# Performance work log

Hardware: AMD Instinct MI355X
Metric: run time of the kernel (lower is better)

The kernel has to match this reference:

```python
import jax, jax.numpy as jnp
import numpy as np

DIM = 2048
NH = 16
HD = DIM // NH  # 128


def setup_inputs() -> dict:
    key = jax.random.key(0)
    ks = jax.random.split(key, 9)
    s_in = 1.0 / np.sqrt(DIM)
    inp = {
        "x": jax.random.normal(ks[0], (2, 2048, DIM), dtype=jnp.float32),
        # torch Linear weights stored as (out, in); we keep (in, out) for x @ W
        "wq": jax.random.uniform(ks[1], (DIM, DIM), jnp.float32, -s_in, s_in),
        "bq": jax.random.uniform(ks[2], (DIM,), jnp.float32, -s_in, s_in),
        "wk": jax.random.uniform(ks[3], (DIM, HD), jnp.float32, -s_in, s_in),
        "bk": jax.random.uniform(ks[4], (HD,), jnp.float32, -s_in, s_in),
        "wv": jax.random.uniform(ks[5], (DIM, HD), jnp.float32, -s_in, s_in),
        "bv": jax.random.uniform(ks[6], (HD,), jnp.float32, -s_in, s_in),
        "wo": jax.random.uniform(ks[7], (DIM, DIM), jnp.float32, -s_in, s_in),
        "bo": jax.random.uniform(ks[8], (DIM,), jnp.float32, -s_in, s_in),
    }
    return inp


def reference(x, wq, bq, wk, bk, wv, bv, wo, bo):
    bs, sl, dim = x.shape
    q = x @ wq + bq                      # [b, s, dim]
    k = x @ wk + bk                      # [b, s, hd] (single shared KV head)
    v = x @ wv + bv                      # [b, s, hd]
    q = q.reshape(bs, sl, NH, HD)        # [b, s, h, hd]
    scale = 1.0 / np.sqrt(HD).astype(np.float32)
    # scores: broadcast single KV head over all query heads
    attn = jnp.einsum('bshd,btd->bhst', q, k) * scale   # [b, h, s, s]
    att = jax.nn.softmax(attn, axis=-1)
    o = jnp.einsum('bhst,btd->bshd', att, v)            # [b, s, h, hd]
    o = o.reshape(bs, sl, dim)
    return o @ wo + bo
```

## Files before the change

### kernel.cpp

```cpp
#include <hip/hip_runtime.h>
#include <hip/hip_bf16.h>
#include <math.h>

#define DIM 2048
#define NH 16
#define HD 128
#define BATCH 2
#define SEQ 2048
#define TOKENS (BATCH * SEQ)
#define NQKV (DIM + 2 * HD)

typedef __attribute__((ext_vector_type(8))) _Float16 f16x8;
typedef __attribute__((ext_vector_type(4))) float f32x4;
typedef unsigned short u16;

__device__ __forceinline__ u16 f2h(float f) {
    union { _Float16 h; u16 u; } v; v.h = (_Float16)f; return v.u;
}
__device__ __forceinline__ void gll16(const void* g, void* l) {
    __builtin_amdgcn_global_load_lds(
        (const __attribute__((address_space(1))) unsigned int*)g,
        (__attribute__((address_space(3))) unsigned int*)l, 16, 0, 0);
}

#define KIDX(r, c) ((r) * 128 + (((((c) << 1)) ^ (((r) & 7) << 4)) >> 1))
#define VIDX(d, c) ((d) * 64  + (((((c) << 1)) ^ (((d) & 7) << 4)) >> 1))
#define PIDX(row, col) ((row) * 64 + \
    (((((col) << 1)) ^ (((((row) >> 2) & 3) ^ ((row) & 3)) << 5)) >> 1))

__global__ __launch_bounds__(256) void conv_f16(
    const float* __restrict__ in, u16* __restrict__ out)
{
    const int i = blockIdx.x * 256 + threadIdx.x;
    const float4 v = ((const float4*)in)[i];
    ushort4 h;
    h.x = f2h(v.x); h.y = f2h(v.y); h.z = f2h(v.z); h.w = f2h(v.w);
    ((ushort4*)out)[i] = h;
}

__global__ __launch_bounds__(256) void transpose_f16(
    const float* __restrict__ W, u16* __restrict__ T, int K, int N, int rowoff)
{
    __shared__ float tile[32][33];
    const int k0 = blockIdx.x * 32;
    const int n0 = blockIdx.y * 32;
    const int tid = threadIdx.x;
#pragma unroll
    for (int i = 0; i < 4; ++i) {
        const int idx = tid + i * 256;
        const int r = idx >> 5, c = idx & 31;
        tile[r][c] = W[(size_t)(k0 + r) * N + n0 + c];
    }
    __syncthreads();
#pragma unroll
    for (int i = 0; i < 4; ++i) {
        const int idx = tid + i * 256;
        const int r = idx >> 5, c = idx & 31;
        T[(size_t)(rowoff + n0 + r) * K + k0 + c] = f2h(tile[c][r]);
    }
}

__global__ __launch_bounds__(256) void concat_bias(
    const float* __restrict__ bq, const float* __restrict__ bk,
    const float* __restrict__ bv, float* __restrict__ bc)
{
    const int i = blockIdx.x * 256 + threadIdx.x;
    float v;
    if (i < DIM) v = bq[i];
    else if (i < DIM + HD) v = bk[i - DIM];
    else v = bv[i - DIM - HD];
    bc[i] = v;
}

template <int MODE>
__global__ __launch_bounds__(256) void gemm_f16(
    const u16* __restrict__ A, const u16* __restrict__ B,
    const float* __restrict__ bias, float* __restrict__ Cf,
    u16* __restrict__ qdst, u16* __restrict__ kdst, u16* __restrict__ vtdst,
    float scale)
{
    constexpr int BK = 32;
    __shared__ u16 lds[2][2 * 128 * BK];

    const int tid = threadIdx.x;
    const int wid = tid >> 6;
    const int lane = tid & 63;
    const int lr = lane & 15;
    const int lhi = lane >> 4;
    const int wr = wid >> 1, wc = wid & 1;
    const int bm = blockIdx.y * 128;
    const int bn = blockIdx.x * 128;

    f32x4 acc[4][4];
#pragma unroll
    for (int i = 0; i < 4; ++i)
#pragma unroll
        for (int j = 0; j < 4; ++j) acc[i][j] = (f32x4){0.f, 0.f, 0.f, 0.f};

#define STAGE(buf_, k0_)                                                      \
    {                                                                         \
        _Pragma("unroll")                                                     \
        for (int rr = 0; rr < 2; ++rr) {                                      \
            const int slot = rr * 256 + tid;                                  \
            const int row = slot >> 2;                                        \
            const int gch = ((slot & 3) ^ ((row >> 1) & 3)) * 8;              \
            char* lbase = (char*)lds[buf_] + (size_t)(rr * 256 + wid * 64) * 16; \
            gll16(A + (size_t)(bm + row) * DIM + (k0_) + gch, lbase);         \
            gll16(B + (size_t)(bn + row) * DIM + (k0_) + gch, lbase + 8192);  \
        }                                                                     \
    }

    STAGE(0, 0);
    __syncthreads();

    int cur = 0;
    for (int k0 = 0; k0 < DIM; k0 += BK) {
        if (k0 + BK < DIM) STAGE(cur ^ 1, k0 + BK);

        f16x8 a[4], b[4];
#pragma unroll
        for (int i = 0; i < 4; ++i) {
            const int mrow = wr * 64 + i * 16 + lr;
            const int nrow = wc * 64 + i * 16 + lr;
            a[i] = *(const f16x8*)&lds[cur][mrow * BK + ((lhi ^ ((mrow >> 1) & 3)) * 8)];
            b[i] = *(const f16x8*)&lds[cur][4096 + nrow * BK + ((lhi ^ ((nrow >> 1) & 3)) * 8)];
        }
        __builtin_amdgcn_s_setprio(1);
#pragma unroll
        for (int i = 0; i < 4; ++i)
#pragma unroll
            for (int j = 0; j < 4; ++j)
                acc[i][j] = __builtin_amdgcn_mfma_f32_16x16x32_f16(a[i], b[j], acc[i][j], 0, 0, 0);
        __builtin_amdgcn_s_setprio(0);
        __syncthreads();
        cur ^= 1;
    }
#undef STAGE

    const float alpha = (MODE == 0 && bn < DIM) ? scale : 1.0f;
    float bj[4];
#pragma unroll
    for (int j = 0; j < 4; ++j) bj[j] = bias[bn + wc * 64 + j * 16 + lr];

#pragma unroll
    for (int i = 0; i < 4; ++i) {
#pragma unroll
        for (int j = 0; j < 4; ++j) {
#pragma unroll
            for (int r = 0; r < 4; ++r) {
                const int row = bm + wr * 64 + i * 16 + lhi * 4 + r;
                const int col = bn + wc * 64 + j * 16 + lr;
                const float val = (acc[i][j][r] + bj[j]) * alpha;
                if (MODE == 1) {
                    Cf[(size_t)row * DIM + col] = val;
                } else if (bn < DIM) {
                    qdst[(size_t)row * DIM + col] = f2h(val);
                } else if (bn < DIM + HD) {
                    kdst[(size_t)row * HD + (col - DIM)] = f2h(val);
                } else {
                    vtdst[(size_t)(col - DIM - HD) * TOKENS + row] = f2h(val);
                }
            }
        }
    }
}

__global__ __launch_bounds__(256, 2) void mqa_attn_f16(
    const u16* __restrict__ Q, const u16* __restrict__ Kg,
    const u16* __restrict__ Vtg, u16* __restrict__ Oh)
{
    __shared__ __align__(16) u16 Ks[2][64 * 128];
    __shared__ __align__(16) u16 Vt[2][128 * 64];
    __shared__ __align__(16) u16 Ps[4][32 * 64];

    const int tid = threadIdx.x;
    const int wid = tid >> 6;
    const int lane = tid & 63;
    const int lr = lane & 15;
    const int lhi = lane >> 4;

    const int qt = blockIdx.x;
    const int h  = blockIdx.y;
    const int b  = blockIdx.z;
    const size_t bseq = (size_t)b * SEQ;
    const int q0 = qt * 128 + wid * 32;

    f16x8 qf[2][4];
#pragma unroll
    for (int mt = 0; mt < 2; ++mt) {
        const u16* qrow = Q + (bseq + q0 + mt * 16 + lr) * DIM + (size_t)h * HD;
#pragma unroll
        for (int kk = 0; kk < 4; ++kk)
            qf[mt][kk] = *(const f16x8*)(qrow + kk * 32 + lhi * 8);
    }

    f16x8 ones;
#pragma unroll
    for (int j = 0; j < 8; ++j) ones[j] = (_Float16)1.0f;

    f32x4 o[2][8];
#pragma unroll
    for (int mt = 0; mt < 2; ++mt)
#pragma unroll
        for (int dt = 0; dt < 8; ++dt) o[mt][dt] = (f32x4){0.f, 0.f, 0.f, 0.f};
    float m[2][4], lsum[2][4];
#pragma unroll
    for (int mt = 0; mt < 2; ++mt)
#pragma unroll
        for (int r = 0; r < 4; ++r) { m[mt][r] = -INFINITY; lsum[mt][r] = 0.f; }

#define STAGE_KV(buf_, t0_)                                                   \
    {                                                                         \
        _Pragma("unroll")                                                     \
        for (int i = 0; i < 4; ++i) {                                         \
            const int L = i * 256 + tid;                                      \
            char* kbase = (char*)&Ks[buf_][0] + (size_t)(i * 256 + wid * 64) * 16; \
            char* vbase = (char*)&Vt[buf_][0] + (size_t)(i * 256 + wid * 64) * 16; \
            const int krow = L >> 4, kc = (L & 15) ^ ((L >> 4) & 7);          \
            const int vrow = L >> 3, vc = (L & 7) ^ ((L >> 3) & 7);           \
            gll16(&Kg[(bseq + (t0_) + krow) * HD + kc * 8], kbase);           \
            gll16(&Vtg[(size_t)vrow * TOKENS + bseq + (t0_) + vc * 8], vbase);\
        }                                                                     \
    }

    STAGE_KV(0, 0);
    __syncthreads();

    int cur = 0;
    for (int t0 = 0; t0 < SEQ; t0 += 64) {
        if (t0 + 64 < SEQ) STAGE_KV(cur ^ 1, t0 + 64);

        f32x4 sc[2][4];
#pragma unroll
        for (int mt = 0; mt < 2; ++mt)
#pragma unroll
            for (int ct = 0; ct < 4; ++ct) sc[mt][ct] = (f32x4){0.f, 0.f, 0.f, 0.f};
        __builtin_amdgcn_s_setprio(1);
#pragma unroll
        for (int kk = 0; kk < 4; ++kk)
#pragma unroll
            for (int ct = 0; ct < 4; ++ct) {
                const f16x8 kf = *(const f16x8*)&Ks[cur][KIDX(ct * 16 + lr, kk * 32 + lhi * 8)];
                sc[0][ct] = __builtin_amdgcn_mfma_f32_16x16x32_f16(qf[0][kk], kf, sc[0][ct], 0, 0, 0);
                sc[1][ct] = __builtin_amdgcn_mfma_f32_16x16x32_f16(qf[1][kk], kf, sc[1][ct], 0, 0, 0);
            }
        __builtin_amdgcn_s_setprio(0);

        float al[2][4];
        bool need[2] = {false, false};
#pragma unroll
        for (int mt = 0; mt < 2; ++mt) {
            float pm[4];
#pragma unroll
            for (int r = 0; r < 4; ++r)
                pm[r] = fmaxf(fmaxf(sc[mt][0][r], sc[mt][1][r]),
                              fmaxf(sc[mt][2][r], sc[mt][3][r]));
#pragma unroll
            for (int msk = 1; msk < 16; msk <<= 1)
#pragma unroll
                for (int r = 0; r < 4; ++r)
                    pm[r] = fmaxf(pm[r], __shfl_xor(pm[r], msk, 64));
#pragma unroll
            for (int r = 0; r < 4; ++r) {
                if (pm[r] > m[mt][r] + 8.f) {
                    al[mt][r] = __expf(m[mt][r] - pm[r]);
                    m[mt][r] = pm[r];
                    need[mt] = true;
                } else {
                    al[mt][r] = 1.f;
                }
            }
#pragma unroll
            for (int ct = 0; ct < 4; ++ct)
#pragma unroll
                for (int r = 0; r < 4; ++r)
                    Ps[wid][PIDX(mt * 16 + lhi * 4 + r, ct * 16 + lr)] =
                        f2h(__expf(sc[mt][ct][r] - m[mt][r]));
            if (need[mt]) {
#pragma unroll
                for (int dt = 0; dt < 8; ++dt)
#pragma unroll
                    for (int r = 0; r < 4; ++r)
                        o[mt][dt][r] *= al[mt][r];
            }
        }

        f32x4 lacc[2];
        lacc[0] = (f32x4){0.f, 0.f, 0.f, 0.f};
        lacc[1] = (f32x4){0.f, 0.f, 0.f, 0.f};
        __builtin_amdgcn_s_setprio(1);
#pragma unroll
        for (int kk = 0; kk < 2; ++kk) {
            const f16x8 pa0 = *(const f16x8*)&Ps[wid][PIDX(lr, kk * 32 + lhi * 8)];
            const f16x8 pa1 = *(const f16x8*)&Ps[wid][PIDX(16 + lr, kk * 32 + lhi * 8)];
            lacc[0] = __builtin_amdgcn_mfma_f32_16x16x32_f16(pa0, ones, lacc[0], 0, 0, 0);
            lacc[1] = __builtin_amdgcn_mfma_f32_16x16x32_f16(pa1, ones, lacc[1], 0, 0, 0);
#pragma unroll
            for (int dt = 0; dt < 8; ++dt) {
                const f16x8 vb = *(const f16x8*)&Vt[cur][VIDX(dt * 16 + lr, kk * 32 + lhi * 8)];
                o[0][dt] = __builtin_amdgcn_mfma_f32_16x16x32_f16(pa0, vb, o[0][dt], 0, 0, 0);
                o[1][dt] = __builtin_amdgcn_mfma_f32_16x16x32_f16(pa1, vb, o[1][dt], 0, 0, 0);
            }
        }
        __builtin_amdgcn_s_setprio(0);
#pragma unroll
        for (int mt = 0; mt < 2; ++mt)
#pragma unroll
            for (int r = 0; r < 4; ++r)
                lsum[mt][r] = lsum[mt][r] * al[mt][r] + lacc[mt][r];

        __syncthreads();
        cur ^= 1;
    }
#undef STAGE_KV

#pragma unroll
    for (int mt = 0; mt < 2; ++mt)
#pragma unroll
        for (int r = 0; r < 4; ++r) {
            const float inv = 1.f / lsum[mt][r];
            u16* op = Oh + (bseq + q0 + mt * 16 + lhi * 4 + r) * DIM
                         + (size_t)h * HD + lr;
#pragma unroll
            for (int dt = 0; dt < 8; ++dt)
                op[dt * 16] = f2h(o[mt][dt][r] * inv);
        }
}

extern "C" void kernel_launch(void* const* d_in, const int* in_sizes, int n_in,
                              void* d_out, int out_size, void* d_ws, size_t ws_size,
                              hipStream_t stream) {
    const float* x  = (const float*)d_in[0];
    const float* wq = (const float*)d_in[1];
    const float* bq = (const float*)d_in[2];
    const float* wk = (const float*)d_in[3];
    const float* bk = (const float*)d_in[4];
    const float* wv = (const float*)d_in[5];
    const float* bv = (const float*)d_in[6];
    const float* wo = (const float*)d_in[7];
    const float* bo = (const float*)d_in[8];
    float* out = (float*)d_out;

    char* w = (char*)d_ws;
    u16* xh     = (u16*)w;                 w += (size_t)TOKENS * DIM * 2;
    u16* wcat   = (u16*)w;                 w += (size_t)NQKV * DIM * 2;
    u16* woT    = (u16*)w;                 w += (size_t)DIM * DIM * 2;
    u16* qb     = (u16*)w;                 w += (size_t)TOKENS * DIM * 2;
    u16* kb     = (u16*)w;                 w += (size_t)TOKENS * HD * 2;
    u16* vtb    = (u16*)w;                 w += (size_t)TOKENS * HD * 2;
    float* bc   = (float*)w;               w += 16384;
    u16* Oh = xh;

    const float scale = 0.08838834764831845f;
    const dim3 blk(256);

    conv_f16<<<TOKENS * DIM / 4 / 256, blk, 0, stream>>>(x, xh);
    transpose_f16<<<dim3(DIM / 32, DIM / 32), blk, 0, stream>>>(wq, wcat, DIM, DIM, 0);
    transpose_f16<<<dim3(DIM / 32, HD / 32), blk, 0, stream>>>(wk, wcat, DIM, HD, DIM);
    transpose_f16<<<dim3(DIM / 32, HD / 32), blk, 0, stream>>>(wv, wcat, DIM, HD, DIM + HD);
    transpose_f16<<<dim3(DIM / 32, DIM / 32), blk, 0, stream>>>(wo, woT, DIM, DIM, 0);
    concat_bias<<<NQKV / 256, blk, 0, stream>>>(bq, bk, bv, bc);

    gemm_f16<0><<<dim3(NQKV / 128, TOKENS / 128), blk, 0, stream>>>(
        xh, wcat, bc, nullptr, qb, kb, vtb, scale);

    mqa_attn_f16<<<dim3(SEQ / 128, NH, BATCH), blk, 0, stream>>>(qb, kb, vtb, Oh);

    gemm_f16<1><<<dim3(DIM / 128, TOKENS / 128), blk, 0, stream>>>(
        Oh, woT, bo, out, nullptr, nullptr, nullptr, 1.0f);
}
```

Baseline: 246.0 us.

## Transpose attention MFMAs to keep P in registers via permlane swaps

```diff
diff --git a/kernel.cpp b/kernel.cpp
--- a/kernel.cpp
+++ b/kernel.cpp
@@ -11,8 +11,12 @@
 #define NQKV (DIM + 2 * HD)
 
 typedef __attribute__((ext_vector_type(8))) _Float16 f16x8;
+typedef __attribute__((ext_vector_type(2))) _Float16 f16x2;
 typedef __attribute__((ext_vector_type(4))) float f32x4;
 typedef unsigned short u16;
+typedef unsigned int u32;
+
+typedef union { u32 d[4]; f16x8 v; } frag_u;
 
 __device__ __forceinline__ u16 f2h(float f) {
     union { _Float16 h; u16 u; } v; v.h = (_Float16)f; return v.u;
@@ -25,8 +29,6 @@
 
 #define KIDX(r, c) ((r) * 128 + (((((c) << 1)) ^ (((r) & 7) << 4)) >> 1))
 #define VIDX(d, c) ((d) * 64  + (((((c) << 1)) ^ (((d) & 7) << 4)) >> 1))
-#define PIDX(row, col) ((row) * 64 + \
-    (((((col) << 1)) ^ (((((row) >> 2) & 3) ^ ((row) & 3)) << 5)) >> 1))
 
 __global__ __launch_bounds__(256) void conv_f16(
     const float* __restrict__ in, u16* __restrict__ out)
@@ -171,13 +173,13 @@
 {
     __shared__ __align__(16) u16 Ks[2][64 * 128];
     __shared__ __align__(16) u16 Vt[2][128 * 64];
-    __shared__ __align__(16) u16 Ps[4][32 * 64];
 
     const int tid = threadIdx.x;
     const int wid = tid >> 6;
     const int lane = tid & 63;
     const int lr = lane & 15;
     const int lhi = lane >> 4;
+    const bool l5 = (lhi & 2) != 0;
 
     const int qt = blockIdx.x;
     const int h  = blockIdx.y;
@@ -203,11 +205,8 @@
     for (int mt = 0; mt < 2; ++mt)
 #pragma unroll
         for (int dt = 0; dt < 8; ++dt) o[mt][dt] = (f32x4){0.f, 0.f, 0.f, 0.f};
-    float m[2][4], lsum[2][4];
-#pragma unroll
-    for (int mt = 0; mt < 2; ++mt)
-#pragma unroll
-        for (int r = 0; r < 4; ++r) { m[mt][r] = -INFINITY; lsum[mt][r] = 0.f; }
+    float m[2]    = {-INFINITY, -INFINITY};
+    float lsum[2] = {0.f, 0.f};
 
 #define STAGE_KV(buf_, t0_)                                                   \
     {                                                                         \
@@ -241,48 +240,62 @@
 #pragma unroll
             for (int ct = 0; ct < 4; ++ct) {
                 const f16x8 kf = *(const f16x8*)&Ks[cur][KIDX(ct * 16 + lr, kk * 32 + lhi * 8)];
-                sc[0][ct] = __builtin_amdgcn_mfma_f32_16x16x32_f16(qf[0][kk], kf, sc[0][ct], 0, 0, 0);
-                sc[1][ct] = __builtin_amdgcn_mfma_f32_16x16x32_f16(qf[1][kk], kf, sc[1][ct], 0, 0, 0);
+                sc[0][ct] = __builtin_amdgcn_mfma_f32_16x16x32_f16(kf, qf[0][kk], sc[0][ct], 0, 0, 0);
+                sc[1][ct] = __builtin_amdgcn_mfma_f32_16x16x32_f16(kf, qf[1][kk], sc[1][ct], 0, 0, 0);
             }
         __builtin_amdgcn_s_setprio(0);
 
-        float al[2][4];
-        bool need[2] = {false, false};
+        frag_u pa[2][2];
+        float al[2];
 #pragma unroll
         for (int mt = 0; mt < 2; ++mt) {
-            float pm[4];
-#pragma unroll
-            for (int r = 0; r < 4; ++r)
-                pm[r] = fmaxf(fmaxf(sc[mt][0][r], sc[mt][1][r]),
-                              fmaxf(sc[mt][2][r], sc[mt][3][r]));
-#pragma unroll
-            for (int msk = 1; msk < 16; msk <<= 1)
-#pragma unroll
-                for (int r = 0; r < 4; ++r)
-                    pm[r] = fmaxf(pm[r], __shfl_xor(pm[r], msk, 64));
-#pragma unroll
-            for (int r = 0; r < 4; ++r) {
-                if (pm[r] > m[mt][r] + 8.f) {
-                    al[mt][r] = __expf(m[mt][r] - pm[r]);
-                    m[mt][r] = pm[r];
-                    need[mt] = true;
-                } else {
-                    al[mt][r] = 1.f;
+            float pm = fmaxf(fmaxf(fmaxf(sc[mt][0][0], sc[mt][0][1]),
+                                   fmaxf(sc[mt][0][2], sc[mt][0][3])),
+                             fmaxf(fmaxf(sc[mt][1][0], sc[mt][1][1]),
+                                   fmaxf(sc[mt][1][2], sc[mt][1][3])));
+            pm = fmaxf(pm, fmaxf(fmaxf(fmaxf(sc[mt][2][0], sc[mt][2][1]),
+                                       fmaxf(sc[mt][2][2], sc[mt][2][3])),
+                                 fmaxf(fmaxf(sc[mt][3][0], sc[mt][3][1]),
+                                       fmaxf(sc[mt][3][2], sc[mt][3][3]))));
+            pm = fmaxf(pm, __shfl_xor(pm, 16));
+            pm = fmaxf(pm, __shfl_xor(pm, 32));
+
+            const bool grow = pm > m[mt] + 8.f;
+            al[mt] = 1.f;
+            if (__any(grow)) {
+                if (grow) { al[mt] = __expf(m[mt] - pm); m[mt] = pm; }
+#pragma unroll
+                for (int dt = 0; dt < 8; ++dt)
+#pragma unroll
+                    for (int r = 0; r < 4; ++r)
+                        o[mt][dt][r] *= al[mt];
+            }
+
+            u32 pk[4][2];
+#pragma unroll
+            for (int ct = 0; ct < 4; ++ct) {
+                const float p0 = __expf(sc[mt][ct][0] - m[mt]);
+                const float p1 = __expf(sc[mt][ct][1] - m[mt]);
+                const float p2 = __expf(sc[mt][ct][2] - m[mt]);
+                const float p3 = __expf(sc[mt][ct][3] - m[mt]);
+                pk[ct][0] = __builtin_bit_cast(u32, __builtin_amdgcn_cvt_pkrtz(p0, p1));
+                pk[ct][1] = __builtin_bit_cast(u32, __builtin_amdgcn_cvt_pkrtz(p2, p3));
+            }
+
+#pragma unroll
+            for (int kk = 0; kk < 2; ++kk)
+#pragma unroll
+                for (int p = 0; p < 2; ++p) {
+                    const u32 X = pk[2 * kk + 0][p];
+                    const u32 Y = pk[2 * kk + 1][p];
+                    const u32 sx = __shfl_xor(X, 32);
+                    const u32 sy = __shfl_xor(Y, 32);
+                    const u32 X1 = l5 ? sy : X;
+                    const u32 Y1 = l5 ? Y : sx;
+                    const auto u2 = __builtin_amdgcn_permlane16_swap(X1, Y1, false, false);
+                    pa[mt][kk].d[p]     = u2[0];
+                    pa[mt][kk].d[2 + p] = u2[1];
                 }
-            }
-#pragma unroll
-            for (int ct = 0; ct < 4; ++ct)
-#pragma unroll
-                for (int r = 0; r < 4; ++r)
-                    Ps[wid][PIDX(mt * 16 + lhi * 4 + r, ct * 16 + lr)] =
-                        f2h(__expf(sc[mt][ct][r] - m[mt][r]));
-            if (need[mt]) {
-#pragma unroll
-                for (int dt = 0; dt < 8; ++dt)
-#pragma unroll
-                    for (int r = 0; r < 4; ++r)
-                        o[mt][dt][r] *= al[mt][r];
-            }
         }
 
         f32x4 lacc[2];
@@ -291,23 +304,19 @@
         __builtin_amdgcn_s_setprio(1);
 #pragma unroll
         for (int kk = 0; kk < 2; ++kk) {
-            const f16x8 pa0 = *(const f16x8*)&Ps[wid][PIDX(lr, kk * 32 + lhi * 8)];
-            const f16x8 pa1 = *(const f16x8*)&Ps[wid][PIDX(16 + lr, kk * 32 + lhi * 8)];
-            lacc[0] = __builtin_amdgcn_mfma_f32_16x16x32_f16(pa0, ones, lacc[0], 0, 0, 0);
-            lacc[1] = __builtin_amdgcn_mfma_f32_16x16x32_f16(pa1, ones, lacc[1], 0, 0, 0);
+            lacc[0] = __builtin_amdgcn_mfma_f32_16x16x32_f16(ones, pa[0][kk].v, lacc[0], 0, 0, 0);
+            lacc[1] = __builtin_amdgcn_mfma_f32_16x16x32_f16(ones, pa[1][kk].v, lacc[1], 0, 0, 0);
 #pragma unroll
             for (int dt = 0; dt < 8; ++dt) {
-                const f16x8 vb = *(const f16x8*)&Vt[cur][VIDX(dt * 16 + lr, kk * 32 + lhi * 8)];
-                o[0][dt] = __builtin_amdgcn_mfma_f32_16x16x32_f16(pa0, vb, o[0][dt], 0, 0, 0);
-                o[1][dt] = __builtin_amdgcn_mfma_f32_16x16x32_f16(pa1, vb, o[1][dt], 0, 0, 0);
+                const f16x8 vf = *(const f16x8*)&Vt[cur][VIDX(dt * 16 + lr, kk * 32 + lhi * 8)];
+                o[0][dt] = __builtin_amdgcn_mfma_f32_16x16x32_f16(vf, pa[0][kk].v, o[0][dt], 0, 0, 0);
+                o[1][dt] = __builtin_amdgcn_mfma_f32_16x16x32_f16(vf, pa[1][kk].v, o[1][dt], 0, 0, 0);
             }
         }
         __builtin_amdgcn_s_setprio(0);
 #pragma unroll
         for (int mt = 0; mt < 2; ++mt)
-#pragma unroll
-            for (int r = 0; r < 4; ++r)
-                lsum[mt][r] = lsum[mt][r] * al[mt][r] + lacc[mt][r];
+            lsum[mt] = lsum[mt] * al[mt] + lacc[mt][0];
 
         __syncthreads();
         cur ^= 1;
@@ -315,16 +324,19 @@
 #undef STAGE_KV
 
 #pragma unroll
-    for (int mt = 0; mt < 2; ++mt)
-#pragma unroll
-        for (int r = 0; r < 4; ++r) {
-            const float inv = 1.f / lsum[mt][r];
-            u16* op = Oh + (bseq + q0 + mt * 16 + lhi * 4 + r) * DIM
-                         + (size_t)h * HD + lr;
-#pragma unroll
-            for (int dt = 0; dt < 8; ++dt)
-                op[dt * 16] = f2h(o[mt][dt][r] * inv);
-        }
+    for (int mt = 0; mt < 2; ++mt) {
+        const float inv = 1.f / lsum[mt];
+        const size_t base = (bseq + q0 + mt * 16 + lr) * DIM + (size_t)h * HD + lhi * 4;
+#pragma unroll
+        for (int dt = 0; dt < 8; ++dt) {
+            ushort4 h4;
+            h4.x = f2h(o[mt][dt][0] * inv);
+            h4.y = f2h(o[mt][dt][1] * inv);
+            h4.z = f2h(o[mt][dt][2] * inv);
+            h4.w = f2h(o[mt][dt][3] * inv);
+            *(ushort4*)&Oh[base + dt * 16] = h4;
+        }
+    }
 }
 
 extern "C" void kernel_launch(void* const* d_in, const int* in_sizes, int n_in,
```

Result: faster. 224.6 us (-8.7%).
